# Optimization experiments

Hardware: AMD Instinct MI355X
Metric: run time of the kernel (lower is better)

## Reference

```python
import jax, jax.numpy as jnp
import numpy as np

B, S, D = 4, 1024, 1024
H, DK, DV = 16, 64, 64
LN_EPS = 1e-5

def setup_inputs() -> dict:
    key = jax.random.key(0)
    ks = jax.random.split(key, 8)
    sc_q = 1.0 / np.sqrt(D)
    return {
        "Q": jax.random.normal(ks[0], (B, S, D), jnp.float32),
        "K": jax.random.normal(ks[1], (B, S, D), jnp.float32),
        "V": jax.random.normal(ks[2], (B, S, D), jnp.float32),
        "mask": jnp.zeros((B, S, S), dtype=bool),
        "W_Q": jax.random.normal(ks[3], (D, H * DK), jnp.float32) * sc_q,
        "W_K": jax.random.normal(ks[4], (D, H * DK), jnp.float32) * sc_q,
        "W_V": jax.random.normal(ks[5], (D, H * DV), jnp.float32) * sc_q,
        "W_O": jax.random.normal(ks[6], (H * DV, D), jnp.float32) * (1.0 / np.sqrt(H * DV)),
        "ln_gamma": jnp.ones((D,), jnp.float32),
        "ln_beta": jnp.zeros((D,), jnp.float32),
    }

def reference(Q, K, V, mask, W_Q, W_K, W_V, W_O, ln_gamma, ln_beta):
    residual = Q
    # projections -> [B, H, S, dk/dv]
    q = (Q @ W_Q).reshape(B, S, H, DK).transpose(0, 2, 1, 3)
    k = (K @ W_K).reshape(B, S, H, DK).transpose(0, 2, 1, 3)
    v = (V @ W_V).reshape(B, S, H, DV).transpose(0, 2, 1, 3)
    # scores [B, H, Sq, Sk]
    scores = jnp.einsum('bhqd,bhkd->bhqk', q, k) / jnp.sqrt(jnp.float32(DK))
    scores = jnp.where(mask[:, None, :, :], -jnp.inf, scores)
    # faithful to original: softmax over dim=2 (the QUERY axis)
    attn = jax.nn.softmax(scores, axis=2)
    out = jnp.einsum('bhqk,bhkd->bhqd', attn, v)  # [B, H, Sq, dv]
    out = out.transpose(0, 2, 1, 3).reshape(B, S, H * DV)
    out = out @ W_O + residual
    # LayerNorm over last dim
    mu = jnp.mean(out, axis=-1, keepdims=True)
    var = jnp.var(out, axis=-1, keepdims=True)
    out = (out - mu) * jax.lax.rsqrt(var + LN_EPS) * ln_gamma + ln_beta
    return out, attn
```

## Files before the change

### kernel.cpp

```cpp
#include <hip/hip_runtime.h>
#include <hip/hip_bf16.h>


typedef __bf16 bf16;
typedef bf16 bf16x4 __attribute__((ext_vector_type(4)));
typedef bf16 bf16x8 __attribute__((ext_vector_type(8)));
typedef float f32x4 __attribute__((ext_vector_type(4)));
typedef unsigned char u8x16 __attribute__((ext_vector_type(16)));

#define MFMA(a, b, c) __builtin_amdgcn_mfma_f32_16x16x32_bf16((a), (b), (c), 0, 0, 0)

__device__ __forceinline__ bf16 f2b(float x) { return (bf16)x; }

__device__ __forceinline__ void gl_lds16(const bf16* g, void* l) {
    __builtin_amdgcn_global_load_lds(
        (const __attribute__((address_space(1))) void*)g,
        (__attribute__((address_space(3))) void*)l, 16, 0, 0);
}

__device__ __forceinline__ void wait_lgkm() {
    __builtin_amdgcn_sched_barrier(0);
    asm volatile("s_waitcnt lgkmcnt(0)" ::: "memory");
    __builtin_amdgcn_sched_barrier(0);
}

__global__ __launch_bounds__(256) void k_cvt(
    const float* __restrict__ Q, const float* __restrict__ K, const float* __restrict__ V,
    bf16* __restrict__ Qb, bf16* __restrict__ Kb, bf16* __restrict__ Vb)
{
    const int z = blockIdx.y;
    const float* src = z == 0 ? Q : z == 1 ? K : V;
    bf16* dst = z == 0 ? Qb : z == 1 ? Kb : Vb;
    const float sc = z == 0 ? 0.125f : 1.0f;
    size_t idx = ((size_t)blockIdx.x * 256 + threadIdx.x) * 8;
    const size_t stride = (size_t)gridDim.x * 2048;
    for (; idx < 4194304; idx += stride) {
        const float4 v0 = *(const float4*)(src + idx);
        const float4 v1 = *(const float4*)(src + idx + 4);
        bf16x8 o = { f2b(v0.x * sc), f2b(v0.y * sc), f2b(v0.z * sc), f2b(v0.w * sc),
                     f2b(v1.x * sc), f2b(v1.y * sc), f2b(v1.z * sc), f2b(v1.w * sc) };
        *(bf16x8*)(dst + idx) = o;
    }
}

__global__ __launch_bounds__(256) void k_transpose(
    const float* __restrict__ W0, const float* __restrict__ W1,
    const float* __restrict__ W2, const float* __restrict__ W3,
    bf16* __restrict__ T0, bf16* __restrict__ T1,
    bf16* __restrict__ T2, bf16* __restrict__ T3)
{
    const float* W = blockIdx.z == 0 ? W0 : blockIdx.z == 1 ? W1 : blockIdx.z == 2 ? W2 : W3;
    bf16*        T = blockIdx.z == 0 ? T0 : blockIdx.z == 1 ? T1 : blockIdx.z == 2 ? T2 : T3;
    __shared__ float tile[32][33];
    const int t = threadIdx.x;
    const int r = t >> 3, c = (t & 7) * 4;
    {
        const float4 v = *(const float4*)(W + (size_t)(blockIdx.y * 32 + r) * 1024 + blockIdx.x * 32 + c);
        tile[r][c + 0] = v.x; tile[r][c + 1] = v.y; tile[r][c + 2] = v.z; tile[r][c + 3] = v.w;
    }
    __syncthreads();
    bf16x4 o = { f2b(tile[c + 0][r]), f2b(tile[c + 1][r]), f2b(tile[c + 2][r]), f2b(tile[c + 3][r]) };
    *(bf16x4*)(T + (size_t)(blockIdx.x * 32 + r) * 1024 + blockIdx.y * 32 + c) = o;
}

__global__ __launch_bounds__(256) void k_proj(
    const bf16* __restrict__ Xq, const bf16* __restrict__ Xk, const bf16* __restrict__ Xv,
    const bf16* __restrict__ WTq, const bf16* __restrict__ WTk, const bf16* __restrict__ WTv,
    bf16* __restrict__ qh, bf16* __restrict__ kh, bf16* __restrict__ vTh)
{
    const int z = blockIdx.z;
    const bf16* X  = z == 0 ? Xq : z == 1 ? Xk : Xv;
    const bf16* WT = z == 0 ? WTq : z == 1 ? WTk : WTv;

    __shared__ char AsB[8192];
    __shared__ char BsB[16384];

    const int tid = threadIdx.x;
    const int lane = tid & 63, w = tid >> 6;
    const int lr = lane & 15, lg = lane >> 4;
    const int wm = w >> 1, wn = w & 1;
    const int m0 = blockIdx.y * 64, n0 = blockIdx.x * 128;

    const int lrow = lane >> 3;
    const int swz8 = ((lane & 7) ^ lrow) * 8;
    const bf16* Ab = X  + (size_t)(m0 + w * 8 + lrow) * 1024 + swz8;
    const bf16* Bb = WT + (size_t)(n0 + w * 8 + lrow) * 1024 + swz8;
    char* Alb = AsB + w * 1024;
    char* Blb = BsB + w * 1024;

    f32x4 acc[2][4] = {};

    for (int k0 = 0; k0 < 1024; k0 += 64) {
        gl_lds16(Ab + k0,          Alb);
        gl_lds16(Ab + 32768 + k0,  Alb + 4096);
        #pragma unroll
        for (int i = 0; i < 4; ++i)
            gl_lds16(Bb + (size_t)i * 32768 + k0, Blb + i * 4096);
        __syncthreads();
        #pragma unroll
        for (int ks = 0; ks < 2; ++ks) {
            const int swr = ((ks * 4 + lg) ^ (lr & 7)) << 4;
            bf16x8 a[2], bb[4];
            #pragma unroll
            for (int fm = 0; fm < 2; ++fm)
                a[fm] = *(const bf16x8*)(AsB + (wm * 32 + fm * 16 + lr) * 128 + swr);
            #pragma unroll
            for (int fn = 0; fn < 4; ++fn)
                bb[fn] = *(const bf16x8*)(BsB + (wn * 64 + fn * 16 + lr) * 128 + swr);
            #pragma unroll
            for (int fm = 0; fm < 2; ++fm)
                #pragma unroll
                for (int fn = 0; fn < 4; ++fn)
                    acc[fm][fn] = MFMA(a[fm], bb[fn], acc[fm][fn]);
        }
        __syncthreads();
    }

    if (z < 2) {
        bf16* dst = (z == 0) ? qh : kh;
        #pragma unroll
        for (int fm = 0; fm < 2; ++fm)
            #pragma unroll
            for (int fn = 0; fn < 4; ++fn)
                #pragma unroll
                for (int r = 0; r < 4; ++r) {
                    const int m = m0 + wm * 32 + fm * 16 + lg * 4 + r;
                    const int n = n0 + wn * 64 + fn * 16 + lr;
                    const int b = m >> 10, s = m & 1023, h = n >> 6, d = n & 63;
                    dst[(((size_t)(b * 16 + h)) * 1024 + s) * 64 + d] = f2b(acc[fm][fn][r]);
                }
    } else {
        #pragma unroll
        for (int fm = 0; fm < 2; ++fm)
            #pragma unroll
            for (int fn = 0; fn < 4; ++fn) {
                const int m = m0 + wm * 32 + fm * 16 + lg * 4;
                const int n = n0 + wn * 64 + fn * 16 + lr;
                const int b = m >> 10, s = m & 1023, h = n >> 6, d = n & 63;
                bf16x4 o = { f2b(acc[fm][fn][0]), f2b(acc[fm][fn][1]),
                             f2b(acc[fm][fn][2]), f2b(acc[fm][fn][3]) };
                *(bf16x4*)&vTh[(((size_t)(b * 16 + h)) * 64 + d) * 1024 + s] = o;
            }
    }
}

__global__ __launch_bounds__(256) void k_colsum(
    const bf16* __restrict__ qh, const bf16* __restrict__ kh,
    const unsigned char* __restrict__ mask, float* __restrict__ inv_colsum)
{
    const int bid = blockIdx.x;
    const int wg = (bid & 7) * 256 + (bid >> 3);
    const int bh = wg >> 5;
    const int kk0 = (wg & 31) * 32;
    const int b = bh >> 4;
    const bf16* qb = qh + (size_t)bh * 65536;
    const bf16* kb = kh + (size_t)bh * 65536;
    const unsigned char* mb = mask + (size_t)b * 1048576;

    const int tid = threadIdx.x;
    const int lane = tid & 63, w = tid >> 6;
    const int lr = lane & 15, lg = lane >> 4;

    __shared__ unsigned char Ml[2][128 * 48];
    __shared__ float csum[4][32];

    const int mrow = tid >> 1, mcoff = (tid & 1) * 16;

    bf16x8 bfr[2][2];
    #pragma unroll
    for (int fn = 0; fn < 2; ++fn)
        #pragma unroll
        for (int ks = 0; ks < 2; ++ks)
            bfr[fn][ks] = *(const bf16x8*)(kb + (size_t)(kk0 + fn * 16 + lr) * 64 + ks * 32 + lg * 8);

    *(u8x16*)&Ml[0][mrow * 48 + mcoff] =
        *(const u8x16*)(mb + (size_t)mrow * 1024 + kk0 + mcoff);
    wait_lgkm();

    float colacc[2][4] = {};

    for (int q0 = 0; q0 < 1024; q0 += 128) {
        const int cur = (q0 >> 7) & 1;
        if (q0 + 128 < 1024)
            *(u8x16*)&Ml[cur ^ 1][mrow * 48 + mcoff] =
                *(const u8x16*)(mb + (size_t)(q0 + 128 + mrow) * 1024 + kk0 + mcoff);

        bf16x8 a[2][2];
        #pragma unroll
        for (int fm = 0; fm < 2; ++fm) {
            const int q = q0 + w * 32 + fm * 16 + lr;
            a[fm][0] = *(const bf16x8*)(qb + (size_t)q * 64 + lg * 8);
            a[fm][1] = *(const bf16x8*)(qb + (size_t)q * 64 + 32 + lg * 8);
        }

        #pragma unroll
        for (int fm = 0; fm < 2; ++fm) {
            const int ql = w * 32 + fm * 16 + lr;
            #pragma unroll
            for (int fn = 0; fn < 2; ++fn) {
                f32x4 c = {0.f, 0.f, 0.f, 0.f};
                c = MFMA(bfr[fn][0], a[fm][0], c);
                c = MFMA(bfr[fn][1], a[fm][1], c);
                const unsigned int m4 = *(const unsigned int*)&Ml[cur][ql * 48 + fn * 16 + lg * 4];
                #pragma unroll
                for (int r = 0; r < 4; ++r)
                    colacc[fn][r] += ((m4 >> (8 * r)) & 255u) ? 0.f : __expf(c[r]);
            }
        }
        wait_lgkm();
    }

    #pragma unroll
    for (int fn = 0; fn < 2; ++fn)
        #pragma unroll
        for (int r = 0; r < 4; ++r) {
            float v = colacc[fn][r];
            v += __shfl_xor(v, 1);
            v += __shfl_xor(v, 2);
            v += __shfl_xor(v, 4);
            v += __shfl_xor(v, 8);
            if (lr == 0) csum[w][fn * 16 + lg * 4 + r] = v;
        }
    __syncthreads();
    if (tid < 32) {
        const float s = csum[0][tid] + csum[1][tid] + csum[2][tid] + csum[3][tid];
        inv_colsum[(size_t)bh * 1024 + kk0 + tid] = 1.0f / s;
    }
}

__global__ __launch_bounds__(256) void k_attn(
    const bf16* __restrict__ qh, const bf16* __restrict__ kh, const bf16* __restrict__ vTh,
    const unsigned char* __restrict__ mask, const float* __restrict__ inv_colsum,
    float* __restrict__ attn_out, bf16* __restrict__ attn_head)
{
    const int bid = blockIdx.x;
    const int wg = (bid & 7) * 256 + (bid >> 3);
    const int bh = wg >> 5;
    const int q0 = (wg & 31) * 32;
    const int b = bh >> 4, h = bh & 15;
    const bf16* qb = qh + (size_t)bh * 65536;
    const bf16* kb = kh + (size_t)bh * 65536;
    const bf16* vb = vTh + (size_t)bh * 65536;
    const unsigned char* mb = mask + (size_t)b * 1048576 + (size_t)q0 * 1024;

    const int tid = threadIdx.x;
    const int lane = tid & 63, w = tid >> 6;
    const int lr = lane & 15, lg = lane >> 4;

    __shared__ __align__(16) char smem[17408 + 8192];
    bf16* Pl = (bf16*)smem;
    unsigned char* Mw = (unsigned char*)(smem + 17408) + w * 2048;
    f32x4* red = (f32x4*)smem;
    bf16* Ao = (bf16*)(smem + 17408);

    const int msrow = lane >> 1, msoff = (lane & 1) * 16;

    bf16x8 af[2][2];
    #pragma unroll
    for (int fm = 0; fm < 2; ++fm)
        #pragma unroll
        for (int ks = 0; ks < 2; ++ks)
            af[fm][ks] = *(const bf16x8*)(qb + (size_t)(q0 + fm * 16 + lr) * 64 + ks * 32 + lg * 8);

    *(u8x16*)&Mw[msrow * 32 + msoff] =
        *(const u8x16*)(mb + (size_t)msrow * 1024 + w * 32 + msoff);
    wait_lgkm();

    f32x4 pacc[2][4] = {};

    #pragma unroll
    for (int it = 0; it < 8; ++it) {
        const int kk0 = it << 7;
        const int cur = it & 1;
        bf16* P = Pl + cur * 32 * 136;
        const unsigned char* Mc = Mw + cur * 1024;

        if (it < 7)
            *(u8x16*)&Mw[(cur ^ 1) * 1024 + msrow * 32 + msoff] =
                *(const u8x16*)(mb + (size_t)msrow * 1024 + kk0 + 128 + w * 32 + msoff);

        bf16x8 bfr[2][2];
        #pragma unroll
        for (int fn = 0; fn < 2; ++fn)
            #pragma unroll
            for (int ks = 0; ks < 2; ++ks)
                bfr[fn][ks] = *(const bf16x8*)(kb + (size_t)(kk0 + w * 32 + fn * 16 + lr) * 64 + ks * 32 + lg * 8);

        bf16x8 vv[4];
        #pragma unroll
        for (int fn2 = 0; fn2 < 4; ++fn2)
            vv[fn2] = *(const bf16x8*)(vb + (size_t)(fn2 * 16 + lr) * 1024 + kk0 + w * 32 + lg * 8);

        f32x4 linv[2];
        #pragma unroll
        for (int fn = 0; fn < 2; ++fn)
            linv[fn] = *(const f32x4*)(inv_colsum + (size_t)bh * 1024 + kk0 + w * 32 + fn * 16 + lg * 4);

        #pragma unroll
        for (int fm = 0; fm < 2; ++fm)
            #pragma unroll
            for (int fn = 0; fn < 2; ++fn) {
                f32x4 c = {0.f, 0.f, 0.f, 0.f};
                c = MFMA(bfr[fn][0], af[fm][0], c);
                c = MFMA(bfr[fn][1], af[fm][1], c);
                const int ql = fm * 16 + lr;
                const int kloc = w * 32 + fn * 16 + lg * 4;
                const unsigned int m4 = *(const unsigned int*)&Mc[ql * 32 + fn * 16 + lg * 4];
                bf16x4 pb;
                #pragma unroll
                for (int r = 0; r < 4; ++r)
                    pb[r] = f2b(((m4 >> (8 * r)) & 255u) ? 0.f : __expf(c[r]) * linv[fn][r]);
                *(bf16x4*)&P[ql * 136 + kloc] = pb;
            }

        wait_lgkm();

        #pragma unroll
        for (int fm2 = 0; fm2 < 2; ++fm2) {
            const bf16x8 pa = *(const bf16x8*)&P[(fm2 * 16 + lr) * 136 + w * 32 + lg * 8];
            #pragma unroll
            for (int fn2 = 0; fn2 < 4; ++fn2)
                pacc[fm2][fn2] = MFMA(pa, vv[fn2], pacc[fm2][fn2]);
        }

        {
            const int srow = lane >> 3;
            const int c4 = (lane & 7) * 4;
            #pragma unroll
            for (int rr = 0; rr < 4; ++rr) {
                const int row = srow + rr * 8;
                const uint2 pv = *(const uint2*)&P[row * 136 + w * 32 + c4];
                f32x4 o;
                o[0] = __uint_as_float(pv.x << 16);
                o[1] = __uint_as_float(pv.x & 0xffff0000u);
                o[2] = __uint_as_float(pv.y << 16);
                o[3] = __uint_as_float(pv.y & 0xffff0000u);
                *(f32x4*)(attn_out + ((size_t)bh * 1024 + q0 + row) * 1024 + kk0 + w * 32 + c4) = o;
            }
        }
    }

    __syncthreads();
    if (w >= 2)
        #pragma unroll
        for (int fm2 = 0; fm2 < 2; ++fm2)
            #pragma unroll
            for (int fn2 = 0; fn2 < 4; ++fn2)
                red[(fm2 * 4 + fn2) * 128 + (w - 2) * 64 + lane] = pacc[fm2][fn2];
    __syncthreads();
    if (w < 2)
        #pragma unroll
        for (int fm2 = 0; fm2 < 2; ++fm2)
            #pragma unroll
            for (int fn2 = 0; fn2 < 4; ++fn2)
                pacc[fm2][fn2] += red[(fm2 * 4 + fn2) * 128 + w * 64 + lane];
    __syncthreads();
    if (w == 1)
        #pragma unroll
        for (int fm2 = 0; fm2 < 2; ++fm2)
            #pragma unroll
            for (int fn2 = 0; fn2 < 4; ++fn2)
                red[(fm2 * 4 + fn2) * 128 + lane] = pacc[fm2][fn2];
    __syncthreads();
    if (w == 0)
        #pragma unroll
        for (int fm2 = 0; fm2 < 2; ++fm2)
            #pragma unroll
            for (int fn2 = 0; fn2 < 4; ++fn2) {
                const f32x4 s = pacc[fm2][fn2] + red[(fm2 * 4 + fn2) * 128 + lane];
                #pragma unroll
                for (int r = 0; r < 4; ++r)
                    Ao[(fm2 * 16 + lg * 4 + r) * 72 + fn2 * 16 + lr] = f2b(s[r]);
            }
    __syncthreads();
    {
        const int row = tid >> 3, c8 = (tid & 7) * 8;
        const bf16x8 v = *(const bf16x8*)&Ao[row * 72 + c8];
        *(bf16x8*)(attn_head + ((size_t)b * 1024 + q0 + row) * 1024 + h * 64 + c8) = v;
    }
}

__global__ __launch_bounds__(256) void k_outproj(
    const bf16* __restrict__ Ah, const bf16* __restrict__ WTo,
    const float* __restrict__ Qres, float* __restrict__ proj)
{
    __shared__ char AsB[8192];
    __shared__ char BsB[16384];

    const int tid = threadIdx.x;
    const int lane = tid & 63, w = tid >> 6;
    const int lr = lane & 15, lg = lane >> 4;
    const int wm = w >> 1, wn = w & 1;
    const int m0 = blockIdx.y * 64, n0 = blockIdx.x * 128;

    const int lrow = lane >> 3;
    const int swz8 = ((lane & 7) ^ lrow) * 8;
    const bf16* Ab = Ah  + (size_t)(m0 + w * 8 + lrow) * 1024 + swz8;
    const bf16* Bb = WTo + (size_t)(n0 + w * 8 + lrow) * 1024 + swz8;
    char* Alb = AsB + w * 1024;
    char* Blb = BsB + w * 1024;

    f32x4 acc[2][4] = {};

    for (int k0 = 0; k0 < 1024; k0 += 64) {
        gl_lds16(Ab + k0,         Alb);
        gl_lds16(Ab + 32768 + k0, Alb + 4096);
        #pragma unroll
        for (int i = 0; i < 4; ++i)
            gl_lds16(Bb + (size_t)i * 32768 + k0, Blb + i * 4096);
        __syncthreads();
        #pragma unroll
        for (int ks = 0; ks < 2; ++ks) {
            const int swr = ((ks * 4 + lg) ^ (lr & 7)) << 4;
            bf16x8 a[2], bb[4];
            #pragma unroll
            for (int fm = 0; fm < 2; ++fm)
                a[fm] = *(const bf16x8*)(AsB + (wm * 32 + fm * 16 + lr) * 128 + swr);
            #pragma unroll
            for (int fn = 0; fn < 4; ++fn)
                bb[fn] = *(const bf16x8*)(BsB + (wn * 64 + fn * 16 + lr) * 128 + swr);
            #pragma unroll
            for (int fm = 0; fm < 2; ++fm)
                #pragma unroll
                for (int fn = 0; fn < 4; ++fn)
                    acc[fm][fn] = MFMA(a[fm], bb[fn], acc[fm][fn]);
        }
        __syncthreads();
    }

    #pragma unroll
    for (int fm = 0; fm < 2; ++fm)
        #pragma unroll
        for (int fn = 0; fn < 4; ++fn)
            #pragma unroll
            for (int r = 0; r < 4; ++r) {
                const int m = m0 + wm * 32 + fm * 16 + lg * 4 + r;
                const int n = n0 + wn * 64 + fn * 16 + lr;
                proj[(size_t)m * 1024 + n] = acc[fm][fn][r] + Qres[(size_t)m * 1024 + n];
            }
}

__global__ __launch_bounds__(256) void k_ln(
    const float* __restrict__ proj, const float* __restrict__ gam,
    const float* __restrict__ bet, float* __restrict__ out)
{
    const int row = blockIdx.x;
    const int t = threadIdx.x;
    const int lane = t & 63, w = t >> 6;
    const float4 x = *(const float4*)(proj + (size_t)row * 1024 + t * 4);
    float s = x.x + x.y + x.z + x.w;
    float ss = x.x * x.x + x.y * x.y + x.z * x.z + x.w * x.w;
    #pragma unroll
    for (int o = 1; o < 64; o <<= 1) {
        s += __shfl_xor(s, o);
        ss += __shfl_xor(ss, o);
    }
    __shared__ float rs[4], rss[4];
    if (lane == 0) { rs[w] = s; rss[w] = ss; }
    __syncthreads();
    const float S1 = rs[0] + rs[1] + rs[2] + rs[3];
    const float S2 = rss[0] + rss[1] + rss[2] + rss[3];
    const float mu = S1 * (1.0f / 1024.0f);
    const float rstd = rsqrtf(S2 * (1.0f / 1024.0f) - mu * mu + 1e-5f);
    const float4 gg = *(const float4*)(gam + t * 4);
    const float4 bb = *(const float4*)(bet + t * 4);
    float4 y;
    y.x = (x.x - mu) * rstd * gg.x + bb.x;
    y.y = (x.y - mu) * rstd * gg.y + bb.y;
    y.z = (x.z - mu) * rstd * gg.z + bb.z;
    y.w = (x.w - mu) * rstd * gg.w + bb.w;
    *(float4*)(out + (size_t)row * 1024 + t * 4) = y;
}

extern "C" void kernel_launch(void* const* d_in, const int* in_sizes, int n_in,
                              void* d_out, int out_size, void* d_ws, size_t ws_size,
                              hipStream_t stream)
{
    const float* Q  = (const float*)d_in[0];
    const float* K  = (const float*)d_in[1];
    const float* V  = (const float*)d_in[2];
    const unsigned char* mask = (const unsigned char*)d_in[3];
    const float* W_Q = (const float*)d_in[4];
    const float* W_K = (const float*)d_in[5];
    const float* W_V = (const float*)d_in[6];
    const float* W_O = (const float*)d_in[7];
    const float* gam = (const float*)d_in[8];
    const float* bet = (const float*)d_in[9];

    float* out  = (float*)d_out;
    float* attn = out + (size_t)4 * 1024 * 1024;

    bf16* wsb = (bf16*)d_ws;
    const size_t M1 = 1024 * 1024;
    bf16* WTq = wsb + 0 * M1;
    bf16* WTk = wsb + 1 * M1;
    bf16* WTv = wsb + 2 * M1;
    bf16* WTo = wsb + 3 * M1;
    bf16* qh  = wsb + 4 * M1;
    bf16* kh  = wsb + 8 * M1;
    bf16* vTh = wsb + 12 * M1;
    bf16* Xqb = wsb + 16 * M1;
    bf16* Xkb = wsb + 20 * M1;
    bf16* Xvb = wsb + 24 * M1;
    bf16* Ah  = wsb + 16 * M1;
    float* inv_colsum = (float*)(wsb + 20 * M1);
    float* proj       = inv_colsum + 65536;

    const dim3 blk(256);
    k_cvt<<<dim3(512, 3), blk, 0, stream>>>(Q, K, V, Xqb, Xkb, Xvb);
    k_transpose<<<dim3(32, 32, 4), blk, 0, stream>>>(W_Q, W_K, W_V, W_O, WTq, WTk, WTv, WTo);
    k_proj<<<dim3(8, 64, 3), blk, 0, stream>>>(Xqb, Xkb, Xvb, WTq, WTk, WTv, qh, kh, vTh);
    k_colsum<<<dim3(2048), blk, 0, stream>>>(qh, kh, mask, inv_colsum);
    k_attn<<<dim3(2048), blk, 0, stream>>>(qh, kh, vTh, mask, inv_colsum, attn, Ah);
    k_outproj<<<dim3(8, 64), blk, 0, stream>>>(Ah, WTo, Q, proj);
    k_ln<<<dim3(4096), blk, 0, stream>>>(proj, gam, bet, out);
}
```

Measured before the change: 235.0 us.

## Split column-sum over query halves, merge prep kernels, use nontemporal output stores

The column-sum kernel now launches twice as many blocks, each covering half of the query axis. It writes two partial sums, which the attention kernel adds and inverts with a fast reciprocal. The input-conversion and weight-transpose kernels are merged into one launch. The large attention-probability and LayerNorm output writes now use nontemporal stores to avoid polluting the cache. Together these aim to improve occupancy in the column-sum pass and remove one launch, at the cost of an extra partial-sum load in attention and a fast reciprocal that is slightly less precise.

```diff
diff --git a/kernel.cpp b/kernel.cpp
--- a/kernel.cpp
+++ b/kernel.cpp
@@ -24,43 +24,44 @@
     __builtin_amdgcn_sched_barrier(0);
 }
 
-__global__ __launch_bounds__(256) void k_cvt(
+__global__ __launch_bounds__(256) void k_pre(
     const float* __restrict__ Q, const float* __restrict__ K, const float* __restrict__ V,
-    bf16* __restrict__ Qb, bf16* __restrict__ Kb, bf16* __restrict__ Vb)
-{
-    const int z = blockIdx.y;
-    const float* src = z == 0 ? Q : z == 1 ? K : V;
-    bf16* dst = z == 0 ? Qb : z == 1 ? Kb : Vb;
-    const float sc = z == 0 ? 0.125f : 1.0f;
-    size_t idx = ((size_t)blockIdx.x * 256 + threadIdx.x) * 8;
-    const size_t stride = (size_t)gridDim.x * 2048;
-    for (; idx < 4194304; idx += stride) {
-        const float4 v0 = *(const float4*)(src + idx);
-        const float4 v1 = *(const float4*)(src + idx + 4);
-        bf16x8 o = { f2b(v0.x * sc), f2b(v0.y * sc), f2b(v0.z * sc), f2b(v0.w * sc),
-                     f2b(v1.x * sc), f2b(v1.y * sc), f2b(v1.z * sc), f2b(v1.w * sc) };
-        *(bf16x8*)(dst + idx) = o;
-    }
-}
-
-__global__ __launch_bounds__(256) void k_transpose(
     const float* __restrict__ W0, const float* __restrict__ W1,
     const float* __restrict__ W2, const float* __restrict__ W3,
+    bf16* __restrict__ Qb, bf16* __restrict__ Kb, bf16* __restrict__ Vb,
     bf16* __restrict__ T0, bf16* __restrict__ T1,
     bf16* __restrict__ T2, bf16* __restrict__ T3)
 {
-    const float* W = blockIdx.z == 0 ? W0 : blockIdx.z == 1 ? W1 : blockIdx.z == 2 ? W2 : W3;
-    bf16*        T = blockIdx.z == 0 ? T0 : blockIdx.z == 1 ? T1 : blockIdx.z == 2 ? T2 : T3;
+    const int z = blockIdx.y;
     __shared__ float tile[32][33];
-    const int t = threadIdx.x;
-    const int r = t >> 3, c = (t & 7) * 4;
-    {
-        const float4 v = *(const float4*)(W + (size_t)(blockIdx.y * 32 + r) * 1024 + blockIdx.x * 32 + c);
-        tile[r][c + 0] = v.x; tile[r][c + 1] = v.y; tile[r][c + 2] = v.z; tile[r][c + 3] = v.w;
-    }
-    __syncthreads();
-    bf16x4 o = { f2b(tile[c + 0][r]), f2b(tile[c + 1][r]), f2b(tile[c + 2][r]), f2b(tile[c + 3][r]) };
-    *(bf16x4*)(T + (size_t)(blockIdx.x * 32 + r) * 1024 + blockIdx.y * 32 + c) = o;
+    if (z < 3) {
+        const float* src = z == 0 ? Q : z == 1 ? K : V;
+        bf16* dst = z == 0 ? Qb : z == 1 ? Kb : Vb;
+        const float sc = z == 0 ? 0.125f : 1.0f;
+        size_t idx = ((size_t)blockIdx.x * 256 + threadIdx.x) * 8;
+        const size_t stride = (size_t)gridDim.x * 2048;
+        for (; idx < 4194304; idx += stride) {
+            const float4 v0 = *(const float4*)(src + idx);
+            const float4 v1 = *(const float4*)(src + idx + 4);
+            bf16x8 o = { f2b(v0.x * sc), f2b(v0.y * sc), f2b(v0.z * sc), f2b(v0.w * sc),
+                         f2b(v1.x * sc), f2b(v1.y * sc), f2b(v1.z * sc), f2b(v1.w * sc) };
+            *(bf16x8*)(dst + idx) = o;
+        }
+    } else {
+        const int zz = z - 3;
+        const float* W = zz == 0 ? W0 : zz == 1 ? W1 : zz == 2 ? W2 : W3;
+        bf16*        T = zz == 0 ? T0 : zz == 1 ? T1 : zz == 2 ? T2 : T3;
+        const int bx = blockIdx.x & 31, by = blockIdx.x >> 5;
+        const int t = threadIdx.x;
+        const int r = t >> 3, c = (t & 7) * 4;
+        {
+            const float4 v = *(const float4*)(W + (size_t)(by * 32 + r) * 1024 + bx * 32 + c);
+            tile[r][c + 0] = v.x; tile[r][c + 1] = v.y; tile[r][c + 2] = v.z; tile[r][c + 3] = v.w;
+        }
+        __syncthreads();
+        bf16x4 o = { f2b(tile[c + 0][r]), f2b(tile[c + 1][r]), f2b(tile[c + 2][r]), f2b(tile[c + 3][r]) };
+        *(bf16x4*)(T + (size_t)(bx * 32 + r) * 1024 + by * 32 + c) = o;
+    }
 }
 
 __global__ __launch_bounds__(256) void k_proj(
@@ -146,12 +147,15 @@
 
 __global__ __launch_bounds__(256) void k_colsum(
     const bf16* __restrict__ qh, const bf16* __restrict__ kh,
-    const unsigned char* __restrict__ mask, float* __restrict__ inv_colsum)
+    const unsigned char* __restrict__ mask, float* __restrict__ csp)
 {
     const int bid = blockIdx.x;
-    const int wg = (bid & 7) * 256 + (bid >> 3);
-    const int bh = wg >> 5;
-    const int kk0 = (wg & 31) * 32;
+    const int wg = (bid & 7) * 512 + (bid >> 3);
+    const int bh = wg >> 6;
+    const int t6 = wg & 63;
+    const int kk0 = (t6 >> 1) * 32;
+    const int half = t6 & 1;
+    const int qbase = half * 512;
     const int b = bh >> 4;
     const bf16* qb = qh + (size_t)bh * 65536;
     const bf16* kb = kh + (size_t)bh * 65536;
@@ -174,14 +178,16 @@
             bfr[fn][ks] = *(const bf16x8*)(kb + (size_t)(kk0 + fn * 16 + lr) * 64 + ks * 32 + lg * 8);
 
     *(u8x16*)&Ml[0][mrow * 48 + mcoff] =
-        *(const u8x16*)(mb + (size_t)mrow * 1024 + kk0 + mcoff);
+        *(const u8x16*)(mb + (size_t)(qbase + mrow) * 1024 + kk0 + mcoff);
     wait_lgkm();
 
     float colacc[2][4] = {};
 
-    for (int q0 = 0; q0 < 1024; q0 += 128) {
-        const int cur = (q0 >> 7) & 1;
-        if (q0 + 128 < 1024)
+    #pragma unroll
+    for (int qt = 0; qt < 4; ++qt) {
+        const int q0 = qbase + qt * 128;
+        const int cur = qt & 1;
+        if (qt < 3)
             *(u8x16*)&Ml[cur ^ 1][mrow * 48 + mcoff] =
                 *(const u8x16*)(mb + (size_t)(q0 + 128 + mrow) * 1024 + kk0 + mcoff);
 
@@ -224,13 +230,13 @@
     __syncthreads();
     if (tid < 32) {
         const float s = csum[0][tid] + csum[1][tid] + csum[2][tid] + csum[3][tid];
-        inv_colsum[(size_t)bh * 1024 + kk0 + tid] = 1.0f / s;
+        csp[(size_t)half * 65536 + (size_t)bh * 1024 + kk0 + tid] = s;
     }
 }
 
 __global__ __launch_bounds__(256) void k_attn(
     const bf16* __restrict__ qh, const bf16* __restrict__ kh, const bf16* __restrict__ vTh,
-    const unsigned char* __restrict__ mask, const float* __restrict__ inv_colsum,
+    const unsigned char* __restrict__ mask, const float* __restrict__ csp,
     float* __restrict__ attn_out, bf16* __restrict__ attn_head)
 {
     const int bid = blockIdx.x;
@@ -242,6 +248,8 @@
     const bf16* kb = kh + (size_t)bh * 65536;
     const bf16* vb = vTh + (size_t)bh * 65536;
     const unsigned char* mb = mask + (size_t)b * 1048576 + (size_t)q0 * 1024;
+    const float* c0 = csp + (size_t)bh * 1024;
+    const float* c1 = csp + 65536 + (size_t)bh * 1024;
 
     const int tid = threadIdx.x;
     const int lane = tid & 63, w = tid >> 6;
@@ -293,8 +301,13 @@
 
         f32x4 linv[2];
         #pragma unroll
-        for (int fn = 0; fn < 2; ++fn)
-            linv[fn] = *(const f32x4*)(inv_colsum + (size_t)bh * 1024 + kk0 + w * 32 + fn * 16 + lg * 4);
+        for (int fn = 0; fn < 2; ++fn) {
+            const f32x4 s0 = *(const f32x4*)(c0 + kk0 + w * 32 + fn * 16 + lg * 4);
+            const f32x4 s1 = *(const f32x4*)(c1 + kk0 + w * 32 + fn * 16 + lg * 4);
+            #pragma unroll
+            for (int r = 0; r < 4; ++r)
+                linv[fn][r] = __builtin_amdgcn_rcpf(s0[r] + s1[r]);
+        }
 
         #pragma unroll
         for (int fm = 0; fm < 2; ++fm)
@@ -335,7 +348,8 @@
                 o[1] = __uint_as_float(pv.x & 0xffff0000u);
                 o[2] = __uint_as_float(pv.y << 16);
                 o[3] = __uint_as_float(pv.y & 0xffff0000u);
-                *(f32x4*)(attn_out + ((size_t)bh * 1024 + q0 + row) * 1024 + kk0 + w * 32 + c4) = o;
+                __builtin_nontemporal_store(
+                    o, (f32x4*)(attn_out + ((size_t)bh * 1024 + q0 + row) * 1024 + kk0 + w * 32 + c4));
             }
         }
     }
@@ -464,12 +478,12 @@
     const float rstd = rsqrtf(S2 * (1.0f / 1024.0f) - mu * mu + 1e-5f);
     const float4 gg = *(const float4*)(gam + t * 4);
     const float4 bb = *(const float4*)(bet + t * 4);
-    float4 y;
-    y.x = (x.x - mu) * rstd * gg.x + bb.x;
-    y.y = (x.y - mu) * rstd * gg.y + bb.y;
-    y.z = (x.z - mu) * rstd * gg.z + bb.z;
-    y.w = (x.w - mu) * rstd * gg.w + bb.w;
-    *(float4*)(out + (size_t)row * 1024 + t * 4) = y;
+    f32x4 y;
+    y[0] = (x.x - mu) * rstd * gg.x + bb.x;
+    y[1] = (x.y - mu) * rstd * gg.y + bb.y;
+    y[2] = (x.z - mu) * rstd * gg.z + bb.z;
+    y[3] = (x.w - mu) * rstd * gg.w + bb.w;
+    __builtin_nontemporal_store(y, (f32x4*)(out + (size_t)row * 1024 + t * 4));
 }
 
 extern "C" void kernel_launch(void* const* d_in, const int* in_sizes, int n_in,
@@ -503,15 +517,15 @@
     bf16* Xkb = wsb + 20 * M1;
     bf16* Xvb = wsb + 24 * M1;
     bf16* Ah  = wsb + 16 * M1;
-    float* inv_colsum = (float*)(wsb + 20 * M1);
-    float* proj       = inv_colsum + 65536;
+    float* csp  = (float*)(wsb + 0 * M1);
+    float* proj = (float*)(wsb + 20 * M1);
 
     const dim3 blk(256);
-    k_cvt<<<dim3(512, 3), blk, 0, stream>>>(Q, K, V, Xqb, Xkb, Xvb);
-    k_transpose<<<dim3(32, 32, 4), blk, 0, stream>>>(W_Q, W_K, W_V, W_O, WTq, WTk, WTv, WTo);
+    k_pre<<<dim3(1024, 7), blk, 0, stream>>>(Q, K, V, W_Q, W_K, W_V, W_O,
+                                             Xqb, Xkb, Xvb, WTq, WTk, WTv, WTo);
     k_proj<<<dim3(8, 64, 3), blk, 0, stream>>>(Xqb, Xkb, Xvb, WTq, WTk, WTv, qh, kh, vTh);
-    k_colsum<<<dim3(2048), blk, 0, stream>>>(qh, kh, mask, inv_colsum);
-    k_attn<<<dim3(2048), blk, 0, stream>>>(qh, kh, vTh, mask, inv_colsum, attn, Ah);
+    k_colsum<<<dim3(4096), blk, 0, stream>>>(qh, kh, mask, csp);
+    k_attn<<<dim3(2048), blk, 0, stream>>>(qh, kh, vTh, mask, csp, attn, Ah);
     k_outproj<<<dim3(8, 64), blk, 0, stream>>>(Ah, WTo, Q, proj);
     k_ln<<<dim3(4096), blk, 0, stream>>>(proj, gam, bet, out);
 }
```

Measured after the change: 216.6 us. 7.8% less time.
